# Optimization experiments

Measured on AMD Instinct MI355X. Metric: run time of the kernel, lower is better.

The kernel has to match this reference:

```python
import jax, jax.numpy as jnp
import numpy as np

WEIGHT_SP = 0.1
BANDWIDTH = 0.5
EPS = 1e-5


def _l2_normalize(v, axis, eps=1e-12):
    # matches torch F.normalize(p=2): x / max(||x||, eps)
    n = jnp.sqrt(jnp.sum(v * v, axis=axis, keepdims=True))
    return v / jnp.maximum(n, eps)


def _compute_meshgrid(N, H, W):
    rows = jnp.arange(H, dtype=jnp.float32) / (H + 1)
    cols = jnp.arange(W, dtype=jnp.float32) / (W + 1)
    gr, gc = jnp.meshgrid(rows, cols, indexing="ij")
    grid = jnp.stack([gr, gc])[None]  # (1, 2, H, W)
    return jnp.broadcast_to(grid, (N, 2, H, W))


def _l2_distance(x, y):
    # Faithful to the torch code; its broadcasting is only valid for N == 1.
    N, C, H, W = x.shape
    xv = x.reshape(N, C, -1)
    yv = y.reshape(N, C, -1)
    x_s = jnp.sum(xv ** 2, axis=1)          # (N, HW)
    y_s = jnp.sum(yv ** 2, axis=1)          # (N, HW)
    A = jnp.einsum("nci,ncj->nij", yv, xv)  # (N, HW, HW)
    dist = y_s - 2.0 * A + x_s.T            # same broadcast as torch (N==1)
    dist = jnp.swapaxes(dist, 1, 2)         # transpose(1,2); reshape is no-op
    return jnp.maximum(dist, 0.0)


def _cosine_distance(x, y):
    y_mu = jnp.mean(y, axis=(0, 2, 3), keepdims=True)   # (1, C, 1, 1)
    xn = _l2_normalize(x - y_mu, axis=1)
    yn = _l2_normalize(y - y_mu, axis=1)
    N, C = x.shape[:2]
    xn = xn.reshape(N, C, -1)
    yn = yn.reshape(N, C, -1)
    cos = jnp.einsum("nci,ncj->nij", xn, yn)            # (N, HW, HW)
    return 1.0 - cos


def _relative_distance(dist, eps=1e-5):
    dmin = jnp.min(dist, axis=2, keepdims=True)
    return dist / (dmin + eps)


def _compute_cx(dist_tilde, bandwidth):
    w = jnp.exp((1.0 - dist_tilde) / bandwidth)
    return w / jnp.sum(w, axis=2, keepdims=True)


def setup_inputs() -> dict:
    key = jax.random.key(0)
    k1, k2 = jax.random.split(key)
    x = jax.random.normal(k1, (1, 512, 80, 80), dtype=jnp.float32)
    y = jax.random.normal(k2, (1, 512, 80, 80), dtype=jnp.float32)
    return {"x": x, "y": y}


def reference(x, y):
    N, C, H, W = x.shape
    # spatial branch
    grid = _compute_meshgrid(N, H, W)
    cx_sp = _compute_cx(_relative_distance(_l2_distance(grid, grid), 1e-5), BANDWIDTH)
    # feature branch (loss_type == 'cosine')
    cx_feat = _compute_cx(_relative_distance(_cosine_distance(x, y), EPS), BANDWIDTH)
    cx_combine = (1.0 - WEIGHT_SP) * cx_feat + WEIGHT_SP * cx_sp
    k_max = jnp.max(cx_combine, axis=2, keepdims=True)  # (N, HW, 1)
    cx = jnp.mean(k_max, axis=1)                        # (N, 1)
    return jnp.mean(-jnp.log(cx + EPS))
```

## Files before the change

kernel.cpp:

```cpp
#include <hip/hip_runtime.h>
#include <hip/hip_bf16.h>
#include <math.h>

#define HW 6400
#define NC 512
#define NH 80
#define NW 80
#define NCH 25
#define NSLOT 50
#define NCYS 8
#define JCH 256
#define TI 128
#define BK 64
#define NT16 400

typedef __attribute__((ext_vector_type(8))) short short8;
typedef __attribute__((ext_vector_type(4))) float v4f;

#define MU_OFF    0
#define ACC_OFF   512
#define GMAXP_OFF (ACC_OFF + 64)
#define GDIAG_OFF (GMAXP_OFF + HW*NSLOT)
#define ZP_OFF    (GDIAG_OFF + HW)
#define F32_FLOATS (ZP_OFF + HW*NSLOT)
#define XB_BYTE   ((size_t)(((F32_FLOATS*4) + 255) & ~255))
#define YB_BYTE   (XB_BYTE + (size_t)HW*NC*2)
#define G_BYTE    (YB_BYTE + (size_t)HW*NC*2)
#define G_BYTES   ((size_t)NT16 * NT16 * 256)

typedef __attribute__((address_space(1))) unsigned int uint_g;
typedef __attribute__((address_space(3))) unsigned int uint_l;
__device__ __forceinline__ void gload16(const void* g, void* l) {
    __builtin_amdgcn_global_load_lds((const uint_g*)g, (uint_l*)l, 16, 0, 0);
}

__global__ void k_mu(const float* __restrict__ y, float* __restrict__ mu) {
    int c = blockIdx.x;
    const float4* yc4 = (const float4*)(y + (size_t)c * HW);
    float s = 0.f;
    for (int i = threadIdx.x; i < HW / 4; i += 256) {
        float4 v = yc4[i];
        s += (v.x + v.y) + (v.z + v.w);
    }
    __shared__ float red[256];
    red[threadIdx.x] = s;
    __syncthreads();
    for (int off = 128; off > 0; off >>= 1) {
        if (threadIdx.x < off) red[threadIdx.x] += red[threadIdx.x + off];
        __syncthreads();
    }
    if (threadIdx.x == 0) mu[c] = red[0] * (1.0f / HW);
}

__global__ void k_sumsq(const float* __restrict__ x, const float* __restrict__ y,
                        const float* __restrict__ mu,
                        float* __restrict__ psx, float* __restrict__ psy) {
    int i = blockIdx.x * 256 + threadIdx.x;
    int c0 = blockIdx.y * 64;
    float sx = 0.f, sy = 0.f;
    for (int c = c0; c < c0 + 64; ++c) {
        float m = mu[c];
        float dx = x[(size_t)c * HW + i] - m;
        float dy = y[(size_t)c * HW + i] - m;
        sx = fmaf(dx, dx, sx);
        sy = fmaf(dy, dy, sy);
    }
    psx[(size_t)blockIdx.y * HW + i] = sx;
    psy[(size_t)blockIdx.y * HW + i] = sy;
}

__global__ void k_transpose(const float* __restrict__ x, const float* __restrict__ y,
                            const float* __restrict__ mu,
                            const float* __restrict__ psx, const float* __restrict__ psy,
                            unsigned short* __restrict__ xb, unsigned short* __restrict__ yb) {
    __shared__ float tile[64 * 65];
    __shared__ float ssinv[64];
    const int t = threadIdx.x;
    const int i0 = blockIdx.x * 64;
    const int c0 = blockIdx.y * 64;
    const int z = blockIdx.z;
    const float* src = z ? y : x;
    const float* ps  = z ? psy : psx;
    unsigned short* dst = z ? yb : xb;

    if (t < 64) {
        float s = 0.f;
        #pragma unroll
        for (int p = 0; p < 8; ++p) s += ps[(size_t)p * HW + i0 + t];
        ssinv[t] = 1.0f / fmaxf(sqrtf(s), 1e-12f);
    }
    __syncthreads();
    #pragma unroll
    for (int it = 0; it < 4; ++it) {
        int cl = it * 16 + (t >> 4);
        int p0 = (t & 15) * 4;
        float4 v = *(const float4*)(src + (size_t)(c0 + cl) * HW + i0 + p0);
        float m = mu[c0 + cl];
        tile[(p0 + 0) * 65 + cl] = (v.x - m) * ssinv[p0 + 0];
        tile[(p0 + 1) * 65 + cl] = (v.y - m) * ssinv[p0 + 1];
        tile[(p0 + 2) * 65 + cl] = (v.z - m) * ssinv[p0 + 2];
        tile[(p0 + 3) * 65 + cl] = (v.w - m) * ssinv[p0 + 3];
    }
    __syncthreads();
    #pragma unroll
    for (int it = 0; it < 2; ++it) {
        int il = t >> 2;
        int seg = (t & 3) + it * 4;
        unsigned int pk[4];
        #pragma unroll
        for (int p = 0; p < 4; ++p) {
            float v0 = tile[il * 65 + seg * 8 + p * 2];
            float v1 = tile[il * 65 + seg * 8 + p * 2 + 1];
            __hip_bfloat16 h0 = __float2bfloat16(v0);
            __hip_bfloat16 h1 = __float2bfloat16(v1);
            unsigned short u0 = *reinterpret_cast<unsigned short*>(&h0);
            unsigned short u1 = *reinterpret_cast<unsigned short*>(&h1);
            pk[p] = (unsigned int)u0 | ((unsigned int)u1 << 16);
        }
        uint4 val = make_uint4(pk[0], pk[1], pk[2], pk[3]);
        *(uint4*)&dst[(size_t)(i0 + il) * NC + c0 + seg * 8] = val;
    }
}

__device__ __forceinline__ void rmax_epilogue(float (&rmax)[16], float* gmaxp,
                                              int i0, int wr, int wc, int lr, int lg) {
    #pragma unroll
    for (int u = 0; u < 16; ++u) {
        float v = rmax[u];
        v = fmaxf(v, __shfl_xor(v, 1));
        v = fmaxf(v, __shfl_xor(v, 2));
        v = fmaxf(v, __shfl_xor(v, 4));
        v = fmaxf(v, __shfl_xor(v, 8));
        if (lr == 0) {
            int row = i0 + wr * 64 + (u >> 2) * 16 + lg * 4 + (u & 3);
            gmaxp[(size_t)row * NSLOT + blockIdx.y * 2 + wc] = v;
        }
    }
}

template <typename F>
__device__ __forceinline__ void gemm_driver(const unsigned short* __restrict__ Xb,
                                            const unsigned short* __restrict__ Yb,
                                            F&& consume) {
    __shared__ char sA[TI * BK * 2];
    __shared__ char sB[TI * BK * 2];
    const int t = threadIdx.x;
    const int w = t >> 6, l = t & 63;
    const int wr = w >> 1, wc = w & 1;
    const int lr = l & 15, lg = l >> 4;
    const int i0 = blockIdx.x * TI;
    const int jbase = blockIdx.y * JCH;

    int aoff[4][2], boff[4][2];
    #pragma unroll
    for (int mt = 0; mt < 4; ++mt) {
        int row = wr * 64 + mt * 16 + lr;
        #pragma unroll
        for (int ks = 0; ks < 2; ++ks) {
            int seg = ks * 4 + lg;
            aoff[mt][ks] = row * 128 + ((seg ^ (row & 7)) * 16);
        }
    }
    #pragma unroll
    for (int nt = 0; nt < 4; ++nt) {
        int row = wc * 64 + nt * 16 + lr;
        #pragma unroll
        for (int ks = 0; ks < 2; ++ks) {
            int seg = ks * 4 + lg;
            boff[nt][ks] = row * 128 + ((seg ^ (row & 7)) * 16);
        }
    }
    const int strow = l >> 3;
    const int stcol = ((l & 7) ^ strow) * 8;
    char* dA0 = sA + (w * 4 + 0) * 1024;
    char* dA1 = sA + (w * 4 + 1) * 1024;
    char* dA2 = sA + (w * 4 + 2) * 1024;
    char* dA3 = sA + (w * 4 + 3) * 1024;
    char* dB0 = sB + (w * 4 + 0) * 1024;
    char* dB1 = sB + (w * 4 + 1) * 1024;
    char* dB2 = sB + (w * 4 + 2) * 1024;
    char* dB3 = sB + (w * 4 + 3) * 1024;
    const unsigned short* ga = Xb + (size_t)(i0 + w * 32 + strow) * NC + stcol;
    const unsigned short* gb0 = Yb + (size_t)(jbase + w * 32 + strow) * NC + stcol;

    #pragma unroll 1
    for (int jt = 0; jt < JCH; jt += TI) {
        const unsigned short* gb = gb0 + (size_t)jt * NC;
        v4f acc[4][4];
        #pragma unroll
        for (int mt = 0; mt < 4; ++mt)
            #pragma unroll
            for (int nt = 0; nt < 4; ++nt)
                acc[mt][nt] = (v4f){0.f, 0.f, 0.f, 0.f};

        #pragma unroll 1
        for (int kt = 0; kt < NC; kt += BK) {
            __syncthreads();
            gload16(ga + kt,           dA0);
            gload16(ga + 8  * NC + kt, dA1);
            gload16(ga + 16 * NC + kt, dA2);
            gload16(ga + 24 * NC + kt, dA3);
            gload16(gb + kt,           dB0);
            gload16(gb + 8  * NC + kt, dB1);
            gload16(gb + 16 * NC + kt, dB2);
            gload16(gb + 24 * NC + kt, dB3);
            __syncthreads();
            #pragma unroll
            for (int ks = 0; ks < 2; ++ks) {
                short8 af[4], bf[4];
                #pragma unroll
                for (int mt = 0; mt < 4; ++mt) af[mt] = *(const short8*)&sA[aoff[mt][ks]];
                #pragma unroll
                for (int nt = 0; nt < 4; ++nt) bf[nt] = *(const short8*)&sB[boff[nt][ks]];
                #pragma unroll
                for (int mt = 0; mt < 4; ++mt)
                    #pragma unroll
                    for (int nt = 0; nt < 4; ++nt)
                        acc[mt][nt] = __builtin_amdgcn_mfma_f32_16x16x32_bf16(
                            af[mt], bf[nt], acc[mt][nt], 0, 0, 0);
            }
        }
        consume(acc, jt);
    }
}

__global__ __launch_bounds__(256, 2) void k_pass1s(const unsigned short* __restrict__ Xb,
                                                   const unsigned short* __restrict__ Yb,
                                                   float* __restrict__ gmaxp,
                                                   float* __restrict__ gdiag,
                                                   unsigned int* __restrict__ G1) {
    const int t = threadIdx.x;
    const int w = t >> 6, l = t & 63;
    const int wr = w >> 1, wc = w & 1;
    const int lr = l & 15, lg = l >> 4;
    const int i0 = blockIdx.x * TI;
    const int jbase = blockIdx.y * JCH;
    float rmax[16];
    #pragma unroll
    for (int u = 0; u < 16; ++u) rmax[u] = -3.0e38f;

    gemm_driver(Xb, Yb, [&](v4f (&acc)[4][4], int jt) {
        const bool diagblk = (jbase + jt == i0);
        #pragma unroll
        for (int mt = 0; mt < 4; ++mt) {
            size_t rbase = (size_t)(i0 / 16 + wr * 4 + mt) * (NT16 * 64);
            #pragma unroll
            for (int nt = 0; nt < 4; ++nt) {
                int ct = (jbase + jt) / 16 + wc * 4 + nt;
                float g0 = acc[mt][nt][0];
                float g1 = acc[mt][nt][1];
                float g2 = acc[mt][nt][2];
                float g3 = acc[mt][nt][3];
                rmax[mt * 4 + 0] = fmaxf(rmax[mt * 4 + 0], g0);
                rmax[mt * 4 + 1] = fmaxf(rmax[mt * 4 + 1], g1);
                rmax[mt * 4 + 2] = fmaxf(rmax[mt * 4 + 2], g2);
                rmax[mt * 4 + 3] = fmaxf(rmax[mt * 4 + 3], g3);
                unsigned int pk = __builtin_amdgcn_cvt_pk_fp8_f32(g0, g1, 0, false);
                pk = __builtin_amdgcn_cvt_pk_fp8_f32(g2, g3, pk, true);
                G1[rbase + (size_t)ct * 64 + l] = pk;
                if (diagblk) {
                    int rowb = i0 + wr * 64 + mt * 16 + lg * 4;
                    int col = jbase + jt + wc * 64 + nt * 16 + lr;
                    if (col == rowb + 0) gdiag[col] = g0;
                    if (col == rowb + 1) gdiag[col] = g1;
                    if (col == rowb + 2) gdiag[col] = g2;
                    if (col == rowb + 3) gdiag[col] = g3;
                }
            }
        }
    });
    rmax_epilogue(rmax, gmaxp, i0, wr, wc, lr, lg);
}

__global__ __launch_bounds__(256) void k_pass2s(const unsigned int* __restrict__ G1,
                                                const float* __restrict__ gmaxp,
                                                float* __restrict__ zp) {
    const int t = threadIdx.x;
    const int w = t >> 6, l = t & 63;
    const int lr = l & 15, lg = l >> 4;
    const int rt = blockIdx.x * 4 + w;
    const int cy = blockIdx.y;

    float m = -3.0e38f;
    {
        int row = rt * 16 + lr;
        #pragma unroll
        for (int k = 0; k < 13; ++k) {
            int s = lg + 4 * k;
            if (s < NSLOT) m = fmaxf(m, gmaxp[(size_t)row * NSLOT + s]);
        }
        m = fmaxf(m, __shfl_xor(m, 16));
        m = fmaxf(m, __shfl_xor(m, 32));
    }
    float inv_lr = 1.0f / ((1.0f - m) + 1e-5f);
    float c1[4], c2[4];
    #pragma unroll
    for (int r = 0; r < 4; ++r) {
        float iv = __shfl(inv_lr, lg * 4 + r);
        c2[r] = 2.0f * iv;
        c1[r] = 2.0f - 2.0f * iv;
    }

    const unsigned int* base = G1 + (size_t)rt * (NT16 * 64) + l;
    float zs[4] = {0.f, 0.f, 0.f, 0.f};
    #pragma unroll 4
    for (int ct = cy * 50; ct < cy * 50 + 50; ++ct) {
        unsigned int v = base[(size_t)ct * 64];
        float g0 = __builtin_amdgcn_cvt_f32_fp8(v, 0);
        float g1 = __builtin_amdgcn_cvt_f32_fp8(v, 1);
        float g2 = __builtin_amdgcn_cvt_f32_fp8(v, 2);
        float g3 = __builtin_amdgcn_cvt_f32_fp8(v, 3);
        zs[0] += __expf(fmaf(c2[0], g0, c1[0]));
        zs[1] += __expf(fmaf(c2[1], g1, c1[1]));
        zs[2] += __expf(fmaf(c2[2], g2, c1[2]));
        zs[3] += __expf(fmaf(c2[3], g3, c1[3]));
    }
    #pragma unroll
    for (int r = 0; r < 4; ++r) {
        float z = zs[r];
        z += __shfl_xor(z, 1);
        z += __shfl_xor(z, 2);
        z += __shfl_xor(z, 4);
        z += __shfl_xor(z, 8);
        if (lr == 0) {
            int row = rt * 16 + lg * 4 + r;
            zp[(size_t)row * NCYS + cy] = z;
        }
    }
}

__global__ void k_kmax_s(const float* __restrict__ zp, const float* __restrict__ gdiag,
                         const float* __restrict__ gmaxp, float* __restrict__ accum,
                         int* __restrict__ counter, float* __restrict__ out) {
    int i = blockIdx.x * 256 + threadIdx.x;
    float Z = 0.f, gmax = -3.0e38f;
    #pragma unroll
    for (int s = 0; s < NCYS; ++s) Z += zp[(size_t)i * NCYS + s];
    #pragma unroll
    for (int s = 0; s < NSLOT; ++s) gmax = fmaxf(gmax, gmaxp[(size_t)i * NSLOT + s]);
    float dmin = 1.0f - gmax;
    float inv = 1.0f / (dmin + 1e-5f);
    float wmx = __expf(2.0f - 2.0f * dmin * inv);
    float wii = __expf(2.0f - 2.0f * (1.0f - gdiag[i]) * inv);
    float invZ = 1.0f / Z;
    float kmax = fmaxf(0.9f * wmx * invZ, 0.9f * wii * invZ + 0.1f);

    __shared__ float red[256];
    red[threadIdx.x] = kmax;
    __syncthreads();
    for (int off = 128; off > 0; off >>= 1) {
        if (threadIdx.x < off) red[threadIdx.x] += red[threadIdx.x + off];
        __syncthreads();
    }
    if (threadIdx.x == 0) {
        atomicAdd(accum, red[0]);
        __threadfence();
        int n = atomicAdd(counter, 1);
        if (n == (int)gridDim.x - 1) {
            float total = atomicAdd(accum, 0.0f);
            out[0] = -logf(total * (1.0f / HW) + 1e-5f);
        }
    }
}

__global__ __launch_bounds__(256, 2) void k_pass1(const unsigned short* __restrict__ Xb,
                                                  const unsigned short* __restrict__ Yb,
                                                  float* __restrict__ gmaxp) {
    const int t = threadIdx.x;
    const int w = t >> 6, l = t & 63;
    const int wr = w >> 1, wc = w & 1;
    const int lr = l & 15, lg = l >> 4;
    const int i0 = blockIdx.x * TI;
    float rmax[16];
    #pragma unroll
    for (int u = 0; u < 16; ++u) rmax[u] = -3.0e38f;
    gemm_driver(Xb, Yb, [&](v4f (&acc)[4][4], int jt) {
        (void)jt;
        #pragma unroll
        for (int mt = 0; mt < 4; ++mt)
            #pragma unroll
            for (int r = 0; r < 4; ++r) {
                float mm = acc[mt][0][r];
                #pragma unroll
                for (int nt = 1; nt < 4; ++nt) mm = fmaxf(mm, acc[mt][nt][r]);
                rmax[mt * 4 + r] = fmaxf(rmax[mt * 4 + r], mm);
            }
    });
    rmax_epilogue(rmax, gmaxp, i0, wr, wc, lr, lg);
}

__global__ void k_invd(const float* __restrict__ gmaxp, float* __restrict__ invd) {
    int i = blockIdx.x * 256 + threadIdx.x;
    float m = -3.0e38f;
    #pragma unroll
    for (int s = 0; s < NSLOT; ++s) m = fmaxf(m, gmaxp[(size_t)i * NSLOT + s]);
    invd[i] = 1.0f / ((1.0f - m) + 1e-5f);
}

__global__ __launch_bounds__(256, 2) void k_pass2(const unsigned short* __restrict__ Xb,
                                                  const unsigned short* __restrict__ Yb,
                                                  const float* __restrict__ invd,
                                                  float* __restrict__ zp) {
    const int t = threadIdx.x;
    const int w = t >> 6, l = t & 63;
    const int wr = w >> 1, wc = w & 1;
    const int lr = l & 15, lg = l >> 4;
    const int i0 = blockIdx.x * TI;
    float zs[16], c1[16], c2[16];
    #pragma unroll
    for (int u = 0; u < 16; ++u) {
        int row = i0 + wr * 64 + (u >> 2) * 16 + lg * 4 + (u & 3);
        float inv = invd[row];
        c2[u] = 2.0f * inv;
        c1[u] = 2.0f - 2.0f * inv;
        zs[u] = 0.f;
    }
    gemm_driver(Xb, Yb, [&](v4f (&acc)[4][4], int jt) {
        (void)jt;
        #pragma unroll
        for (int mt = 0; mt < 4; ++mt)
            #pragma unroll
            for (int r = 0; r < 4; ++r) {
                int u = mt * 4 + r;
                float s = 0.f;
                #pragma unroll
                for (int nt = 0; nt < 4; ++nt)
                    s += __expf(fmaf(c2[u], acc[mt][nt][r], c1[u]));
                zs[u] += s;
            }
    });
    #pragma unroll
    for (int u = 0; u < 16; ++u) {
        float z = zs[u];
        z += __shfl_xor(z, 1);
        z += __shfl_xor(z, 2);
        z += __shfl_xor(z, 4);
        z += __shfl_xor(z, 8);
        if (lr == 0) {
            int row = i0 + wr * 64 + (u >> 2) * 16 + lg * 4 + (u & 3);
            zp[(size_t)row * NSLOT + blockIdx.y * 2 + wc] = z;
        }
    }
}

__global__ void k_kmax(const float* __restrict__ zp, const float* __restrict__ gmaxp,
                       const unsigned short* __restrict__ Xb, const unsigned short* __restrict__ Yb,
                       float* __restrict__ accum, int* __restrict__ counter,
                       float* __restrict__ out) {
    int i = blockIdx.x * 256 + threadIdx.x;
    float Z = 0.f, gmax = -3.0e38f;
    #pragma unroll
    for (int s = 0; s < NSLOT; ++s) {
        Z += zp[(size_t)i * NSLOT + s];
        gmax = fmaxf(gmax, gmaxp[(size_t)i * NSLOT + s]);
    }
    float gii = 0.f;
    const uint2* xr = (const uint2*)(Xb + (size_t)i * NC);
    const uint2* yr = (const uint2*)(Yb + (size_t)i * NC);
    for (int c4 = 0; c4 < NC / 4; ++c4) {
        uint2 xa = xr[c4], ya = yr[c4];
        float x0 = __uint_as_float((xa.x & 0xFFFFu) << 16), y0 = __uint_as_float((ya.x & 0xFFFFu) << 16);
        float x1 = __uint_as_float(xa.x & 0xFFFF0000u),     y1 = __uint_as_float(ya.x & 0xFFFF0000u);
        float x2 = __uint_as_float((xa.y & 0xFFFFu) << 16), y2 = __uint_as_float((ya.y & 0xFFFFu) << 16);
        float x3 = __uint_as_float(xa.y & 0xFFFF0000u),     y3 = __uint_as_float(ya.y & 0xFFFF0000u);
        gii = fmaf(x0, y0, gii); gii = fmaf(x1, y1, gii);
        gii = fmaf(x2, y2, gii); gii = fmaf(x3, y3, gii);
    }
    float dmin = 1.0f - gmax;
    float inv = 1.0f / (dmin + 1e-5f);
    float wmx = __expf(2.0f - 2.0f * dmin * inv);
    float wii = __expf(2.0f - 2.0f * (1.0f - gii) * inv);
    float invZ = 1.0f / Z;
    float kmax = fmaxf(0.9f * wmx * invZ, 0.9f * wii * invZ + 0.1f);

    __shared__ float red[256];
    red[threadIdx.x] = kmax;
    __syncthreads();
    for (int off = 128; off > 0; off >>= 1) {
        if (threadIdx.x < off) red[threadIdx.x] += red[threadIdx.x + off];
        __syncthreads();
    }
    if (threadIdx.x == 0) {
        atomicAdd(accum, red[0]);
        __threadfence();
        int n = atomicAdd(counter, 1);
        if (n == (int)gridDim.x - 1) {
            float total = atomicAdd(accum, 0.0f);
            out[0] = -logf(total * (1.0f / HW) + 1e-5f);
        }
    }
}

extern "C" void kernel_launch(void* const* d_in, const int* in_sizes, int n_in,
                              void* d_out, int out_size, void* d_ws, size_t ws_size,
                              hipStream_t stream) {
    const float* x = (const float*)d_in[0];
    const float* y = (const float*)d_in[1];
    float* out = (float*)d_out;
    float* ws = (float*)d_ws;

    float* mu    = ws + MU_OFF;
    float* accum = ws + ACC_OFF;
    int*   counter = (int*)(accum + 1);
    float* gmaxp = ws + GMAXP_OFF;
    float* psx   = ws + GMAXP_OFF;
    float* psy   = ws + GMAXP_OFF + 8 * HW;
    float* gdiag = ws + GDIAG_OFF;
    float* zp    = ws + ZP_OFF;
    unsigned short* Xb = (unsigned short*)((char*)d_ws + XB_BYTE);
    unsigned short* Yb = (unsigned short*)((char*)d_ws + YB_BYTE);
    unsigned int*   G1 = (unsigned int*)((char*)d_ws + G_BYTE);

    const bool bigws = ws_size >= (G_BYTE + G_BYTES);

    hipMemsetAsync(accum, 0, 64 * sizeof(float), stream);

    hipLaunchKernelGGL(k_mu, dim3(NC), dim3(256), 0, stream, y, mu);
    hipLaunchKernelGGL(k_sumsq, dim3(HW / 256, NC / 64), dim3(256), 0, stream, x, y, mu, psx, psy);
    hipLaunchKernelGGL(k_transpose, dim3(HW / 64, NC / 64, 2), dim3(256), 0, stream,
                       x, y, mu, psx, psy, Xb, Yb);

    dim3 grid(HW / TI, NCH);
    if (bigws) {
        hipLaunchKernelGGL(k_pass1s, grid, dim3(256), 0, stream, Xb, Yb, gmaxp, gdiag, G1);
        hipLaunchKernelGGL(k_pass2s, dim3(NT16 / 4, NCYS), dim3(256), 0, stream, G1, gmaxp, zp);
        hipLaunchKernelGGL(k_kmax_s, dim3(HW / 256), dim3(256), 0, stream, zp, gdiag, gmaxp,
                           accum, counter, out);
    } else {
        hipLaunchKernelGGL(k_pass1, grid, dim3(256), 0, stream, Xb, Yb, gmaxp);
        hipLaunchKernelGGL(k_invd, dim3(HW / 256), dim3(256), 0, stream, gmaxp, gdiag);
        hipLaunchKernelGGL(k_pass2, grid, dim3(256), 0, stream, Xb, Yb, gdiag, zp);
        hipLaunchKernelGGL(k_kmax, dim3(HW / 256), dim3(256), 0, stream, zp, gmaxp, Xb, Yb,
                           accum, counter, out);
    }
}
```

Before: 156.2 us.

## Fuse sum-of-squares into transpose, vectorize fp8 G1 layout, fold memset into k_mu

The separate k_sumsq and k_transpose kernels become one k_prep kernel. Each block computes the per-pixel norms over all 512 channels, then normalizes, transposes and converts to bf16 in 64-channel chunks. The accumulator memset moves into k_mu, which removes one launch. The fp8 G1 matrix is re-laid out so each lane stores and loads 16-byte uint4 groups of four 16-column tiles, and pass2 uses half as many column splits (NCYS 8→4). The trade-off is that k_prep has only 200 blocks and reads each input twice, so it may under-occupy the GPU and rely on L2 hits.

```diff
diff --git a/kernel.cpp b/kernel.cpp
--- a/kernel.cpp
+++ b/kernel.cpp
@@ -8,11 +8,12 @@
 #define NW 80
 #define NCH 25
 #define NSLOT 50
-#define NCYS 8
+#define NCYS 4
 #define JCH 256
 #define TI 128
 #define BK 64
 #define NT16 400
+#define NCG 100
 
 typedef __attribute__((ext_vector_type(8))) short short8;
 typedef __attribute__((ext_vector_type(4))) float v4f;
@@ -34,7 +35,9 @@
     __builtin_amdgcn_global_load_lds((const uint_g*)g, (uint_l*)l, 16, 0, 0);
 }
 
-__global__ void k_mu(const float* __restrict__ y, float* __restrict__ mu) {
+__global__ void k_mu(const float* __restrict__ y, float* __restrict__ mu,
+                     float* __restrict__ acczero) {
+    if (blockIdx.x == 0 && threadIdx.x < 64) acczero[threadIdx.x] = 0.f;
     int c = blockIdx.x;
     const float4* yc4 = (const float4*)(y + (size_t)c * HW);
     float s = 0.f;
@@ -52,73 +55,80 @@
     if (threadIdx.x == 0) mu[c] = red[0] * (1.0f / HW);
 }
 
-__global__ void k_sumsq(const float* __restrict__ x, const float* __restrict__ y,
-                        const float* __restrict__ mu,
-                        float* __restrict__ psx, float* __restrict__ psy) {
-    int i = blockIdx.x * 256 + threadIdx.x;
-    int c0 = blockIdx.y * 64;
-    float sx = 0.f, sy = 0.f;
-    for (int c = c0; c < c0 + 64; ++c) {
-        float m = mu[c];
-        float dx = x[(size_t)c * HW + i] - m;
-        float dy = y[(size_t)c * HW + i] - m;
-        sx = fmaf(dx, dx, sx);
-        sy = fmaf(dy, dy, sy);
-    }
-    psx[(size_t)blockIdx.y * HW + i] = sx;
-    psy[(size_t)blockIdx.y * HW + i] = sy;
-}
-
-__global__ void k_transpose(const float* __restrict__ x, const float* __restrict__ y,
-                            const float* __restrict__ mu,
-                            const float* __restrict__ psx, const float* __restrict__ psy,
-                            unsigned short* __restrict__ xb, unsigned short* __restrict__ yb) {
+__global__ void k_prep(const float* __restrict__ x, const float* __restrict__ y,
+                       const float* __restrict__ mu,
+                       unsigned short* __restrict__ xb, unsigned short* __restrict__ yb) {
+    __shared__ float smu[NC];
+    __shared__ float part[64][17];
+    __shared__ float ssinv[64];
     __shared__ float tile[64 * 65];
-    __shared__ float ssinv[64];
     const int t = threadIdx.x;
     const int i0 = blockIdx.x * 64;
-    const int c0 = blockIdx.y * 64;
-    const int z = blockIdx.z;
+    const int z = blockIdx.y;
     const float* src = z ? y : x;
-    const float* ps  = z ? psy : psx;
     unsigned short* dst = z ? yb : xb;
 
+    for (int c = t; c < NC; c += 256) smu[c] = mu[c];
+    __syncthreads();
+
+    const int p0 = (t & 15) * 4;
+    const int g  = t >> 4;
+    float a0 = 0.f, a1 = 0.f, a2 = 0.f, a3 = 0.f;
+    #pragma unroll 2
+    for (int ch = 0; ch < 8; ++ch) {
+        #pragma unroll
+        for (int it = 0; it < 4; ++it) {
+            int cl = ch * 64 + it * 16 + g;
+            float m = smu[cl];
+            float4 v = *(const float4*)(src + (size_t)cl * HW + i0 + p0);
+            float d0 = v.x - m, d1 = v.y - m, d2 = v.z - m, d3 = v.w - m;
+            a0 = fmaf(d0, d0, a0); a1 = fmaf(d1, d1, a1);
+            a2 = fmaf(d2, d2, a2); a3 = fmaf(d3, d3, a3);
+        }
+    }
+    part[p0 + 0][g] = a0; part[p0 + 1][g] = a1;
+    part[p0 + 2][g] = a2; part[p0 + 3][g] = a3;
+    __syncthreads();
     if (t < 64) {
         float s = 0.f;
         #pragma unroll
-        for (int p = 0; p < 8; ++p) s += ps[(size_t)p * HW + i0 + t];
+        for (int k = 0; k < 16; ++k) s += part[t][k];
         ssinv[t] = 1.0f / fmaxf(sqrtf(s), 1e-12f);
     }
     __syncthreads();
-    #pragma unroll
-    for (int it = 0; it < 4; ++it) {
-        int cl = it * 16 + (t >> 4);
-        int p0 = (t & 15) * 4;
-        float4 v = *(const float4*)(src + (size_t)(c0 + cl) * HW + i0 + p0);
-        float m = mu[c0 + cl];
-        tile[(p0 + 0) * 65 + cl] = (v.x - m) * ssinv[p0 + 0];
-        tile[(p0 + 1) * 65 + cl] = (v.y - m) * ssinv[p0 + 1];
-        tile[(p0 + 2) * 65 + cl] = (v.z - m) * ssinv[p0 + 2];
-        tile[(p0 + 3) * 65 + cl] = (v.w - m) * ssinv[p0 + 3];
-    }
-    __syncthreads();
-    #pragma unroll
-    for (int it = 0; it < 2; ++it) {
-        int il = t >> 2;
-        int seg = (t & 3) + it * 4;
-        unsigned int pk[4];
-        #pragma unroll
-        for (int p = 0; p < 4; ++p) {
-            float v0 = tile[il * 65 + seg * 8 + p * 2];
-            float v1 = tile[il * 65 + seg * 8 + p * 2 + 1];
-            __hip_bfloat16 h0 = __float2bfloat16(v0);
-            __hip_bfloat16 h1 = __float2bfloat16(v1);
-            unsigned short u0 = *reinterpret_cast<unsigned short*>(&h0);
-            unsigned short u1 = *reinterpret_cast<unsigned short*>(&h1);
-            pk[p] = (unsigned int)u0 | ((unsigned int)u1 << 16);
-        }
-        uint4 val = make_uint4(pk[0], pk[1], pk[2], pk[3]);
-        *(uint4*)&dst[(size_t)(i0 + il) * NC + c0 + seg * 8] = val;
+
+    for (int ch = 0; ch < 8; ++ch) {
+        #pragma unroll
+        for (int it = 0; it < 4; ++it) {
+            int cl = ch * 64 + it * 16 + g;
+            float m = smu[cl];
+            float4 v = *(const float4*)(src + (size_t)cl * HW + i0 + p0);
+            int clo = it * 16 + g;
+            tile[(p0 + 0) * 65 + clo] = (v.x - m) * ssinv[p0 + 0];
+            tile[(p0 + 1) * 65 + clo] = (v.y - m) * ssinv[p0 + 1];
+            tile[(p0 + 2) * 65 + clo] = (v.z - m) * ssinv[p0 + 2];
+            tile[(p0 + 3) * 65 + clo] = (v.w - m) * ssinv[p0 + 3];
+        }
+        __syncthreads();
+        #pragma unroll
+        for (int it = 0; it < 2; ++it) {
+            int il = t >> 2;
+            int seg = (t & 3) + it * 4;
+            unsigned int pk[4];
+            #pragma unroll
+            for (int p = 0; p < 4; ++p) {
+                float v0 = tile[il * 65 + seg * 8 + p * 2];
+                float v1 = tile[il * 65 + seg * 8 + p * 2 + 1];
+                __hip_bfloat16 h0 = __float2bfloat16(v0);
+                __hip_bfloat16 h1 = __float2bfloat16(v1);
+                unsigned short u0 = *reinterpret_cast<unsigned short*>(&h0);
+                unsigned short u1 = *reinterpret_cast<unsigned short*>(&h1);
+                pk[p] = (unsigned int)u0 | ((unsigned int)u1 << 16);
+            }
+            uint4 val = make_uint4(pk[0], pk[1], pk[2], pk[3]);
+            *(uint4*)&dst[(size_t)(i0 + il) * NC + ch * 64 + seg * 8] = val;
+        }
+        __syncthreads();
     }
 }
 
@@ -241,12 +251,12 @@
 
     gemm_driver(Xb, Yb, [&](v4f (&acc)[4][4], int jt) {
         const bool diagblk = (jbase + jt == i0);
+        const int cg = (jbase + jt) / 64 + wc;
         #pragma unroll
         for (int mt = 0; mt < 4; ++mt) {
-            size_t rbase = (size_t)(i0 / 16 + wr * 4 + mt) * (NT16 * 64);
+            unsigned int pks[4];
             #pragma unroll
             for (int nt = 0; nt < 4; ++nt) {
-                int ct = (jbase + jt) / 16 + wc * 4 + nt;
                 float g0 = acc[mt][nt][0];
                 float g1 = acc[mt][nt][1];
                 float g2 = acc[mt][nt][2];
@@ -257,7 +267,7 @@
                 rmax[mt * 4 + 3] = fmaxf(rmax[mt * 4 + 3], g3);
                 unsigned int pk = __builtin_amdgcn_cvt_pk_fp8_f32(g0, g1, 0, false);
                 pk = __builtin_amdgcn_cvt_pk_fp8_f32(g2, g3, pk, true);
-                G1[rbase + (size_t)ct * 64 + l] = pk;
+                pks[nt] = pk;
                 if (diagblk) {
                     int rowb = i0 + wr * 64 + mt * 16 + lg * 4;
                     int col = jbase + jt + wc * 64 + nt * 16 + lr;
@@ -267,6 +277,8 @@
                     if (col == rowb + 3) gdiag[col] = g3;
                 }
             }
+            size_t idx = ((size_t)(i0 / 16 + wr * 4 + mt) * NCG + cg) * 64 + l;
+            ((uint4*)G1)[idx] = make_uint4(pks[0], pks[1], pks[2], pks[3]);
         }
     });
     rmax_epilogue(rmax, gmaxp, i0, wr, wc, lr, lg);
@@ -301,19 +313,23 @@
         c1[r] = 2.0f - 2.0f * iv;
     }
 
-    const unsigned int* base = G1 + (size_t)rt * (NT16 * 64) + l;
+    const uint4* base = (const uint4*)G1 + (size_t)rt * (NCG * 64) + l;
     float zs[4] = {0.f, 0.f, 0.f, 0.f};
-    #pragma unroll 4
-    for (int ct = cy * 50; ct < cy * 50 + 50; ++ct) {
-        unsigned int v = base[(size_t)ct * 64];
-        float g0 = __builtin_amdgcn_cvt_f32_fp8(v, 0);
-        float g1 = __builtin_amdgcn_cvt_f32_fp8(v, 1);
-        float g2 = __builtin_amdgcn_cvt_f32_fp8(v, 2);
-        float g3 = __builtin_amdgcn_cvt_f32_fp8(v, 3);
-        zs[0] += __expf(fmaf(c2[0], g0, c1[0]));
-        zs[1] += __expf(fmaf(c2[1], g1, c1[1]));
-        zs[2] += __expf(fmaf(c2[2], g2, c1[2]));
-        zs[3] += __expf(fmaf(c2[3], g3, c1[3]));
+    #pragma unroll 2
+    for (int cgk = cy * 25; cgk < cy * 25 + 25; ++cgk) {
+        uint4 v = base[(size_t)cgk * 64];
+        #pragma unroll
+        for (int q = 0; q < 4; ++q) {
+            unsigned int pk = (q == 0) ? v.x : (q == 1) ? v.y : (q == 2) ? v.z : v.w;
+            float g0 = __builtin_amdgcn_cvt_f32_fp8(pk, 0);
+            float g1 = __builtin_amdgcn_cvt_f32_fp8(pk, 1);
+            float g2 = __builtin_amdgcn_cvt_f32_fp8(pk, 2);
+            float g3 = __builtin_amdgcn_cvt_f32_fp8(pk, 3);
+            zs[0] += __expf(fmaf(c2[0], g0, c1[0]));
+            zs[1] += __expf(fmaf(c2[1], g1, c1[1]));
+            zs[2] += __expf(fmaf(c2[2], g2, c1[2]));
+            zs[3] += __expf(fmaf(c2[3], g3, c1[3]));
+        }
     }
     #pragma unroll
     for (int r = 0; r < 4; ++r) {
@@ -503,8 +519,6 @@
     float* accum = ws + ACC_OFF;
     int*   counter = (int*)(accum + 1);
     float* gmaxp = ws + GMAXP_OFF;
-    float* psx   = ws + GMAXP_OFF;
-    float* psy   = ws + GMAXP_OFF + 8 * HW;
     float* gdiag = ws + GDIAG_OFF;
     float* zp    = ws + ZP_OFF;
     unsigned short* Xb = (unsigned short*)((char*)d_ws + XB_BYTE);
@@ -513,12 +527,8 @@
 
     const bool bigws = ws_size >= (G_BYTE + G_BYTES);
 
-    hipMemsetAsync(accum, 0, 64 * sizeof(float), stream);
-
-    hipLaunchKernelGGL(k_mu, dim3(NC), dim3(256), 0, stream, y, mu);
-    hipLaunchKernelGGL(k_sumsq, dim3(HW / 256, NC / 64), dim3(256), 0, stream, x, y, mu, psx, psy);
-    hipLaunchKernelGGL(k_transpose, dim3(HW / 64, NC / 64, 2), dim3(256), 0, stream,
-                       x, y, mu, psx, psy, Xb, Yb);
+    hipLaunchKernelGGL(k_mu, dim3(NC), dim3(256), 0, stream, y, mu, accum);
+    hipLaunchKernelGGL(k_prep, dim3(HW / 64, 2), dim3(256), 0, stream, x, y, mu, Xb, Yb);
 
     dim3 grid(HW / TI, NCH);
     if (bigws) {
```

Result: faster. 147.2 us (median of 2 runs) (-5.8%).
